# Kernel tuning notes

Hardware: AMD Instinct MI355X
Metric: run time of the kernel (lower is better)

The kernel has to match this reference:

```python
import jax, jax.numpy as jnp
import numpy as np

NUM_STAB = 1e-3  # numerical_stabilizer for relu kernel


def _relu_feature(x, proj):
    # x: [B, L, H, D], proj: [M, D] -> [B, L, H, M]
    ratio = 1.0 / jnp.sqrt(jnp.asarray(proj.shape[0], x.dtype))
    return jax.nn.relu(ratio * jnp.einsum('blhd,md->blhm', x, proj)) + NUM_STAB


def setup_inputs() -> dict:
    key = jax.random.key(0)
    k1, k2, k3, k4, k5 = jax.random.split(key, 5)
    B, L, H, D, M = 16, 576, 12, 64, 8  # L = length_of_side**2 = 24**2
    return {
        'query': jax.random.normal(k1, (B, L, H, D), dtype=jnp.float32),
        'key': jax.random.normal(k2, (B, L, H, D), dtype=jnp.float32),
        'value': jax.random.normal(k3, (B, L, H, D), dtype=jnp.float32),
        'projection_matrix': jax.random.normal(k4, (M, D), dtype=jnp.float32),
        # RPE mask is nonnegative per-head mixing matrix [H, L, L]
        'mask_matrix': jax.random.uniform(k5, (H, L, L), dtype=jnp.float32),
    }


def reference(query, key, value, projection_matrix, mask_matrix):
    # ReLU kernel features (projection_matrix_type='relu')
    q_prime = _relu_feature(query, projection_matrix)  # [B, L, H, M]
    k_prime = _relu_feature(key, projection_matrix)    # [B, L, H, M]
    B, L, H, M = k_prime.shape
    D = value.shape[-1]

    # D_1[b,l,h,m,d] = k'[b,l,h,m] * v[b,l,h,d], flattened over (m,d)
    D_1 = jnp.einsum('blhm,blhd->blhmd', k_prime, value).reshape(B, L, H, M * D)
    # mask-matrix causal/RPE mixing over the L dimension (per head)
    D_1_hat = jnp.einsum('hij,bjhc->bihc', mask_matrix, D_1).reshape(B, L, H, M, D)
    D_2_hat = jnp.einsum('hij,bjhm->bihm', mask_matrix, k_prime)  # [B, L, H, M]

    av_attention = jnp.einsum('blhm,blhmd->blhd', q_prime, D_1_hat)  # [B, L, H, D]
    ks_sum = jnp.sum(D_2_hat, axis=1)                                # [B, H, M]
    normalizer = jnp.einsum('blhm,bhm->blh', q_prime, ks_sum)        # [B, L, H]
    return av_attention / normalizer[..., None]
```

## Files before the change

### kernel.cpp

```cpp
#include <hip/hip_runtime.h>
#include <hip/hip_bf16.h>


#define B_ 16
#define L_ 576
#define H_ 12
#define D_ 64
#define M_ 8
#define NUM_STAB 1e-3f
#define RATIO 0.35355339059327373f

typedef __attribute__((ext_vector_type(8))) short short8;
typedef __attribute__((ext_vector_type(4))) float f32x4;

union Pack {
    uint4 u4;
    short8 s8;
    uint2 u2[2];
    unsigned u[4];
    unsigned short us[8];
};

__device__ inline unsigned short f2bf(float x) {
    union { float f; unsigned u; } a; a.f = x;
    unsigned r = (a.u + 0x7FFFu + ((a.u >> 16) & 1u)) >> 16;
    return (unsigned short)r;
}
__device__ inline unsigned pk2(float lo, float hi) {
    __hip_bfloat162 h = __float22bfloat162_rn(make_float2(lo, hi));
    union { __hip_bfloat162 b; unsigned u; } c; c.b = h;
    return c.u;
}
__device__ inline float bf2f(unsigned short u) {
    union { unsigned u; float f; } c; c.u = (unsigned)u << 16; return c.f;
}

#define WS_W_OFF  (H_ * L_)
#define WS_QP_OFF (H_ * L_ + B_ * H_ * M_)
#define QP_ELEMS  ((size_t)B_ * H_ * L_ * M_)

__global__ __launch_bounds__(256) void feat_kernel(const float* __restrict__ q,
                                                   const float* __restrict__ k,
                                                   const float* __restrict__ v,
                                                   const float* __restrict__ proj,
                                                   const float* __restrict__ mask,
                                                   unsigned short* __restrict__ qp,
                                                   unsigned short* __restrict__ kp,
                                                   float* __restrict__ cmask,
                                                   unsigned short* __restrict__ vt) {
    __shared__ float cred[4][16];
    const int lc = blockIdx.x, h = blockIdx.y, b = blockIdx.z, t = threadIdx.x;
    const int wv = t >> 6, l = t & 63, r8 = l >> 3, c8 = l & 7;
    const int row = lc * 32 + wv * 8 + r8;

    float4 pj0[8], pj1[8];
#pragma unroll
    for (int m = 0; m < 8; ++m) {
        pj0[m] = *(const float4*)(proj + m * 64 + c8 * 8);
        pj1[m] = *(const float4*)(proj + m * 64 + c8 * 8 + 4);
    }

#pragma unroll
    for (int s = 0; s < 2; ++s) {
        const float* src = s ? k : q;
        unsigned short* dst = s ? kp : qp;
        const float* xp = src + (((size_t)b * L_ + row) * H_ + h) * D_ + c8 * 8;
        float4 x0 = *(const float4*)xp;
        float4 x1 = *(const float4*)(xp + 4);
        x0.x *= RATIO; x0.y *= RATIO; x0.z *= RATIO; x0.w *= RATIO;
        x1.x *= RATIO; x1.y *= RATIO; x1.z *= RATIO; x1.w *= RATIO;
        float p[8];
#pragma unroll
        for (int m = 0; m < 8; ++m) {
            p[m] = x0.x * pj0[m].x + x0.y * pj0[m].y + x0.z * pj0[m].z + x0.w * pj0[m].w
                 + x1.x * pj1[m].x + x1.y * pj1[m].y + x1.z * pj1[m].z + x1.w * pj1[m].w;
        }
#pragma unroll
        for (int st = 1; st <= 4; st <<= 1) {
#pragma unroll
            for (int m = 0; m < 8; ++m) p[m] += __shfl_xor(p[m], st, 64);
        }
        float r = p[0];
        r = (c8 == 1) ? p[1] : r;
        r = (c8 == 2) ? p[2] : r;
        r = (c8 == 3) ? p[3] : r;
        r = (c8 == 4) ? p[4] : r;
        r = (c8 == 5) ? p[5] : r;
        r = (c8 == 6) ? p[6] : r;
        r = (c8 == 7) ? p[7] : r;
        r = fmaxf(r, 0.f) + NUM_STAB;
        dst[((size_t)(b * H_ + h) * L_ + row) * 8 + c8] = f2bf(r);
    }

    {
        const int dv = t >> 2;
        const int jl = (lc & 1) * 32 + (t & 3) * 8;
        const int jt9 = lc >> 1;
        const float* vsrc = v + (((size_t)b * L_ + jt9 * 64 + jl) * H_ + h) * D_ + dv;
        float tv[8];
#pragma unroll
        for (int e = 0; e < 8; ++e) tv[e] = vsrc[(size_t)e * (H_ * D_)];
        Pack pv;
#pragma unroll
        for (int q4 = 0; q4 < 4; ++q4) pv.u[q4] = pk2(tv[2 * q4], tv[2 * q4 + 1]);
        *(uint4*)&vt[((size_t)(b * H_ + h) * 9 + jt9) * 4096 + dv * 64 + jl] = pv.u4;
    }

    if (b < 2) {
        const int c = t & 15, rg = t >> 4;
        const int col0 = lc * 32 + b * 16;
        const float* mb = mask + (size_t)h * L_ * L_ + col0 + c;
        float a = 0.f;
#pragma unroll 4
        for (int k2 = 0; k2 < 36; ++k2) a += mb[(size_t)(rg + 16 * k2) * L_];
        a += __shfl_xor(a, 16, 64);
        a += __shfl_xor(a, 32, 64);
        if ((l >> 4) == 0) cred[wv][c] = a;
        __syncthreads();
        if (t < 16) cmask[h * L_ + col0 + t] = cred[0][t] + cred[1][t] + cred[2][t] + cred[3][t];
    }
}

__global__ __launch_bounds__(64) void wsum_kernel(const unsigned short* __restrict__ kp,
                                                  const float* __restrict__ cmask,
                                                  float* __restrict__ wbuf) {
    const int bh = blockIdx.x, lx = threadIdx.x;
    const int h = bh % H_;
    const unsigned short* kpb = kp + (size_t)bh * L_ * 8;
    const float* cm = cmask + h * L_;
    float a[8] = {0.f, 0.f, 0.f, 0.f, 0.f, 0.f, 0.f, 0.f};
    for (int j = lx; j < L_; j += 64) {
        const float c = cm[j];
        Pack pk; pk.u4 = *(const uint4*)(kpb + (size_t)j * 8);
#pragma unroll
        for (int m = 0; m < 8; ++m) a[m] += c * bf2f(pk.us[m]);
    }
#pragma unroll
    for (int st = 1; st < 64; st <<= 1) {
#pragma unroll
        for (int m = 0; m < 8; ++m) a[m] += __shfl_xor(a[m], st, 64);
    }
    float r = a[0];
    r = (lx == 1) ? a[1] : r;
    r = (lx == 2) ? a[2] : r;
    r = (lx == 3) ? a[3] : r;
    r = (lx == 4) ? a[4] : r;
    r = (lx == 5) ? a[5] : r;
    r = (lx == 6) ? a[6] : r;
    r = (lx == 7) ? a[7] : r;
    if (lx < 8) wbuf[(size_t)bh * 8 + lx] = r;
}

__global__ __launch_bounds__(256, 5) void attn_kernel(const float* __restrict__ mask,
                                                      const unsigned short* __restrict__ qp,
                                                      const unsigned short* __restrict__ kp,
                                                      const unsigned short* __restrict__ vt,
                                                      const float* __restrict__ wbuf,
                                                      float* __restrict__ out) {
    __shared__ __align__(16) unsigned short Sp[4 * 16 * 72];
    __shared__ __align__(16) unsigned short Bt[2][64 * 72];

    const int t = threadIdx.x;
    int id = blockIdx.x;
    const int bhi = id & 7; id >>= 3;
    const int blo = id & 1; id >>= 1;
    const int it = id % 9, h = id / 9;
    const int b = bhi * 2 + blo;
    const int i0 = it * 64;

    const int wv = t >> 6, l = t & 63, c15 = l & 15, kq = l >> 4;
    const int bd = t >> 3, bg = t & 7;
    const int vt_off = bd * 64 + bg * 8;

    const float* maskbase = mask + (size_t)h * L_ * L_ + (size_t)(i0 + 16 * wv + c15) * L_;
    const unsigned short* kpb = kp + (size_t)(b * H_ + h) * L_ * 8;
    const unsigned short* vtb = vt + (size_t)(b * H_ + h) * 9 * 4096;
    unsigned short* SpW = Sp + wv * 16 * 72;

    short8 Bq;
    {
        Pack pk; pk.u4 = make_uint4(0, 0, 0, 0);
        if (kq == 0)
            pk.u4 = *(const uint4*)(qp + ((size_t)(b * H_ + h) * L_ + i0 + 16 * wv + c15) * 8);
        Bq = pk.s8;
    }

    f32x4 acc0 = {0.f, 0.f, 0.f, 0.f}, acc1 = acc0, acc2 = acc0, acc3 = acc0;
    const f32x4 zz = {0.f, 0.f, 0.f, 0.f};

    uint4 a0 = make_uint4(0, 0, 0, 0), a1 = a0, a2 = a0, a3 = a0;
    uint4 vt0, vt1;
    float4 mv0, mv1, mv2, mv3;
    if (kq == 0) {
        a0 = *(const uint4*)(kpb + (size_t)(c15) * 8);
        a1 = *(const uint4*)(kpb + (size_t)(16 + c15) * 8);
        a2 = *(const uint4*)(kpb + (size_t)(32 + c15) * 8);
        a3 = *(const uint4*)(kpb + (size_t)(48 + c15) * 8);
    }
    vt0 = *(const uint4*)(vtb + vt_off);
    vt1 = *(const uint4*)(vtb + 2048 + vt_off);
    mv0 = *(const float4*)(maskbase + 0 + 4 * kq);
    mv1 = *(const float4*)(maskbase + 16 + 4 * kq);
    mv2 = *(const float4*)(maskbase + 32 + 4 * kq);
    mv3 = *(const float4*)(maskbase + 48 + 4 * kq);

    for (int jt = 0; jt < 9; ++jt) {
        const int slab = jt & 1;

        f32x4 s0, s1, s2, s3;
        {
            Pack p0, p1, p2, p3;
            p0.u4 = a0; p1.u4 = a1; p2.u4 = a2; p3.u4 = a3;
            s0 = __builtin_amdgcn_mfma_f32_16x16x32_bf16(p0.s8, Bq, zz, 0, 0, 0);
            s1 = __builtin_amdgcn_mfma_f32_16x16x32_bf16(p1.s8, Bq, zz, 0, 0, 0);
            s2 = __builtin_amdgcn_mfma_f32_16x16x32_bf16(p2.s8, Bq, zz, 0, 0, 0);
            s3 = __builtin_amdgcn_mfma_f32_16x16x32_bf16(p3.s8, Bq, zz, 0, 0, 0);
        }

        *(uint4*)&Bt[slab][bd * 72 + bg * 8] = vt0;
        *(uint4*)&Bt[slab][(bd + 32) * 72 + bg * 8] = vt1;

        {
            uint2 st2;
            st2.x = pk2(s0[0] * mv0.x, s0[1] * mv0.y);
            st2.y = pk2(s0[2] * mv0.z, s0[3] * mv0.w);
            *(uint2*)&SpW[c15 * 72 + 0 + 4 * kq] = st2;
            st2.x = pk2(s1[0] * mv1.x, s1[1] * mv1.y);
            st2.y = pk2(s1[2] * mv1.z, s1[3] * mv1.w);
            *(uint2*)&SpW[c15 * 72 + 16 + 4 * kq] = st2;
            st2.x = pk2(s2[0] * mv2.x, s2[1] * mv2.y);
            st2.y = pk2(s2[2] * mv2.z, s2[3] * mv2.w);
            *(uint2*)&SpW[c15 * 72 + 32 + 4 * kq] = st2;
            st2.x = pk2(s3[0] * mv3.x, s3[1] * mv3.y);
            st2.y = pk2(s3[2] * mv3.z, s3[3] * mv3.w);
            *(uint2*)&SpW[c15 * 72 + 48 + 4 * kq] = st2;
        }

        __syncthreads();

        {
            const int jn = (jt < 8) ? jt + 1 : 0;
            const int j0n = jn * 64;
            if (kq == 0) {
                a0 = *(const uint4*)(kpb + (size_t)(j0n + c15) * 8);
                a1 = *(const uint4*)(kpb + (size_t)(j0n + 16 + c15) * 8);
                a2 = *(const uint4*)(kpb + (size_t)(j0n + 32 + c15) * 8);
                a3 = *(const uint4*)(kpb + (size_t)(j0n + 48 + c15) * 8);
            }
            vt0 = *(const uint4*)(vtb + (size_t)jn * 4096 + vt_off);
            vt1 = *(const uint4*)(vtb + (size_t)jn * 4096 + 2048 + vt_off);
            mv0 = *(const float4*)(maskbase + j0n + 0 + 4 * kq);
            mv1 = *(const float4*)(maskbase + j0n + 16 + 4 * kq);
            mv2 = *(const float4*)(maskbase + j0n + 32 + 4 * kq);
            mv3 = *(const float4*)(maskbase + j0n + 48 + 4 * kq);
        }

        {
            short8 As0 = *(const short8*)&SpW[c15 * 72 + kq * 8];
            short8 As1 = *(const short8*)&SpW[c15 * 72 + 32 + kq * 8];
            const unsigned short* bp0 = &Bt[slab][c15 * 72 + kq * 8];
            const unsigned short* bp1 = bp0 + 16 * 72;
            const unsigned short* bp2 = bp0 + 32 * 72;
            const unsigned short* bp3 = bp0 + 48 * 72;
            acc0 = __builtin_amdgcn_mfma_f32_16x16x32_bf16(As0, *(const short8*)bp0, acc0, 0, 0, 0);
            acc0 = __builtin_amdgcn_mfma_f32_16x16x32_bf16(As1, *(const short8*)(bp0 + 32), acc0, 0, 0, 0);
            acc1 = __builtin_amdgcn_mfma_f32_16x16x32_bf16(As0, *(const short8*)bp1, acc1, 0, 0, 0);
            acc1 = __builtin_amdgcn_mfma_f32_16x16x32_bf16(As1, *(const short8*)(bp1 + 32), acc1, 0, 0, 0);
            acc2 = __builtin_amdgcn_mfma_f32_16x16x32_bf16(As0, *(const short8*)bp2, acc2, 0, 0, 0);
            acc2 = __builtin_amdgcn_mfma_f32_16x16x32_bf16(As1, *(const short8*)(bp2 + 32), acc2, 0, 0, 0);
            acc3 = __builtin_amdgcn_mfma_f32_16x16x32_bf16(As0, *(const short8*)bp3, acc3, 0, 0, 0);
            acc3 = __builtin_amdgcn_mfma_f32_16x16x32_bf16(As1, *(const short8*)(bp3 + 32), acc3, 0, 0, 0);
        }
    }

    const float* wp = wbuf + (size_t)(b * H_ + h) * 8;
    const float4 w0 = *(const float4*)wp;
    const float4 w1 = *(const float4*)(wp + 4);
    Pack pq;
    pq.u4 = *(const uint4*)(qp + ((size_t)(b * H_ + h) * L_ + i0 + 16 * wv + c15) * 8);
    float n = bf2f(pq.us[0]) * w0.x + bf2f(pq.us[1]) * w0.y +
              bf2f(pq.us[2]) * w0.z + bf2f(pq.us[3]) * w0.w +
              bf2f(pq.us[4]) * w1.x + bf2f(pq.us[5]) * w1.y +
              bf2f(pq.us[6]) * w1.z + bf2f(pq.us[7]) * w1.w;
    float iv[4];
#pragma unroll
    for (int r = 0; r < 4; ++r) iv[r] = 1.0f / __shfl(n, 4 * kq + r, 64);

    float* ob = out + (((size_t)b * L_ + i0 + 16 * wv + 4 * kq) * H_ + h) * D_ + c15;
    const f32x4 aa[4] = {acc0, acc1, acc2, acc3};
#pragma unroll
    for (int di = 0; di < 4; ++di)
#pragma unroll
        for (int r = 0; r < 4; ++r)
            ob[(size_t)r * (H_ * D_) + 16 * di] = aa[di][r] * iv[r];
}

extern "C" void kernel_launch(void* const* d_in, const int* in_sizes, int n_in,
                              void* d_out, int out_size, void* d_ws, size_t ws_size,
                              hipStream_t stream) {
    const float* q    = (const float*)d_in[0];
    const float* k    = (const float*)d_in[1];
    const float* v    = (const float*)d_in[2];
    const float* proj = (const float*)d_in[3];
    const float* mask = (const float*)d_in[4];
    float* out = (float*)d_out;

    float* ws = (float*)d_ws;
    float* cmask = ws;
    float* wbuf  = ws + WS_W_OFF;
    unsigned short* qp_w = (unsigned short*)(ws + WS_QP_OFF);
    unsigned short* kp_w = qp_w + QP_ELEMS;
    unsigned short* vt_w = kp_w + QP_ELEMS;

    feat_kernel<<<dim3(L_ / 32, H_, B_), 256, 0, stream>>>(q, k, v, proj, mask, qp_w, kp_w, cmask, vt_w);
    wsum_kernel<<<B_ * H_, 64, 0, stream>>>(kp_w, cmask, wbuf);
    attn_kernel<<<1728, 256, 0, stream>>>(mask, qp_w, kp_w, vt_w, wbuf, out);
}
```

Measured before the change: 192.6 us.

## Load V fragments directly from global into registers, drop shared staging and barrier

The V tile was previously staged through a double-buffered shared-memory slab with a block-wide barrier each iteration. Now each lane loads its MFMA B-operand fragments for V straight from global memory into registers and prefetches the next tile. This removes the per-iteration __syncthreads and the LDS traffic for V. The cost is more registers (occupancy hint lowered from 5 to 4) and V tiles reloaded redundantly by each of the four waves instead of once per block.

```diff
diff --git a/kernel.cpp b/kernel.cpp
--- a/kernel.cpp
+++ b/kernel.cpp
@@ -151,14 +151,13 @@
     if (lx < 8) wbuf[(size_t)bh * 8 + lx] = r;
 }
 
-__global__ __launch_bounds__(256, 5) void attn_kernel(const float* __restrict__ mask,
+__global__ __launch_bounds__(256, 4) void attn_kernel(const float* __restrict__ mask,
                                                       const unsigned short* __restrict__ qp,
                                                       const unsigned short* __restrict__ kp,
                                                       const unsigned short* __restrict__ vt,
                                                       const float* __restrict__ wbuf,
                                                       float* __restrict__ out) {
     __shared__ __align__(16) unsigned short Sp[4 * 16 * 72];
-    __shared__ __align__(16) unsigned short Bt[2][64 * 72];
 
     const int t = threadIdx.x;
     int id = blockIdx.x;
@@ -169,12 +168,10 @@
     const int i0 = it * 64;
 
     const int wv = t >> 6, l = t & 63, c15 = l & 15, kq = l >> 4;
-    const int bd = t >> 3, bg = t & 7;
-    const int vt_off = bd * 64 + bg * 8;
-
-    const float* maskbase = mask + (size_t)h * L_ * L_ + (size_t)(i0 + 16 * wv + c15) * L_;
+
+    const float* maskbase = mask + (size_t)h * L_ * L_ + (size_t)(i0 + 16 * wv + c15) * L_ + 4 * kq;
     const unsigned short* kpb = kp + (size_t)(b * H_ + h) * L_ * 8;
-    const unsigned short* vtb = vt + (size_t)(b * H_ + h) * 9 * 4096;
+    const unsigned short* vfb = vt + (size_t)(b * H_ + h) * 9 * 4096 + c15 * 64 + kq * 8;
     unsigned short* SpW = Sp + wv * 16 * 72;
 
     short8 Bq;
@@ -189,24 +186,27 @@
     const f32x4 zz = {0.f, 0.f, 0.f, 0.f};
 
     uint4 a0 = make_uint4(0, 0, 0, 0), a1 = a0, a2 = a0, a3 = a0;
-    uint4 vt0, vt1;
-    float4 mv0, mv1, mv2, mv3;
     if (kq == 0) {
         a0 = *(const uint4*)(kpb + (size_t)(c15) * 8);
         a1 = *(const uint4*)(kpb + (size_t)(16 + c15) * 8);
         a2 = *(const uint4*)(kpb + (size_t)(32 + c15) * 8);
         a3 = *(const uint4*)(kpb + (size_t)(48 + c15) * 8);
     }
-    vt0 = *(const uint4*)(vtb + vt_off);
-    vt1 = *(const uint4*)(vtb + 2048 + vt_off);
-    mv0 = *(const float4*)(maskbase + 0 + 4 * kq);
-    mv1 = *(const float4*)(maskbase + 16 + 4 * kq);
-    mv2 = *(const float4*)(maskbase + 32 + 4 * kq);
-    mv3 = *(const float4*)(maskbase + 48 + 4 * kq);
-
+    float4 mv0 = *(const float4*)(maskbase + 0);
+    float4 mv1 = *(const float4*)(maskbase + 16);
+    float4 mv2 = *(const float4*)(maskbase + 32);
+    float4 mv3 = *(const float4*)(maskbase + 48);
+    uint4 vb00 = *(const uint4*)(vfb + 0);
+    uint4 vb01 = *(const uint4*)(vfb + 32);
+    uint4 vb10 = *(const uint4*)(vfb + 1024);
+    uint4 vb11 = *(const uint4*)(vfb + 1024 + 32);
+    uint4 vb20 = *(const uint4*)(vfb + 2048);
+    uint4 vb21 = *(const uint4*)(vfb + 2048 + 32);
+    uint4 vb30 = *(const uint4*)(vfb + 3072);
+    uint4 vb31 = *(const uint4*)(vfb + 3072 + 32);
+
+#pragma unroll 1
     for (int jt = 0; jt < 9; ++jt) {
-        const int slab = jt & 1;
-
         f32x4 s0, s1, s2, s3;
         {
             Pack p0, p1, p2, p3;
@@ -217,8 +217,20 @@
             s3 = __builtin_amdgcn_mfma_f32_16x16x32_bf16(p3.s8, Bq, zz, 0, 0, 0);
         }
 
-        *(uint4*)&Bt[slab][bd * 72 + bg * 8] = vt0;
-        *(uint4*)&Bt[slab][(bd + 32) * 72 + bg * 8] = vt1;
+        const int jn = (jt < 8) ? jt + 1 : 0;
+        const int j0n = jn * 64;
+
+        uint4 na0 = make_uint4(0, 0, 0, 0), na1 = na0, na2 = na0, na3 = na0;
+        if (kq == 0) {
+            na0 = *(const uint4*)(kpb + (size_t)(j0n + c15) * 8);
+            na1 = *(const uint4*)(kpb + (size_t)(j0n + 16 + c15) * 8);
+            na2 = *(const uint4*)(kpb + (size_t)(j0n + 32 + c15) * 8);
+            na3 = *(const uint4*)(kpb + (size_t)(j0n + 48 + c15) * 8);
+        }
+        float4 nmv0 = *(const float4*)(maskbase + j0n + 0);
+        float4 nmv1 = *(const float4*)(maskbase + j0n + 16);
+        float4 nmv2 = *(const float4*)(maskbase + j0n + 32);
+        float4 nmv3 = *(const float4*)(maskbase + j0n + 48);
 
         {
             uint2 st2;
@@ -236,41 +248,36 @@
             *(uint2*)&SpW[c15 * 72 + 48 + 4 * kq] = st2;
         }
 
-        __syncthreads();
-
         {
-            const int jn = (jt < 8) ? jt + 1 : 0;
-            const int j0n = jn * 64;
-            if (kq == 0) {
-                a0 = *(const uint4*)(kpb + (size_t)(j0n + c15) * 8);
-                a1 = *(const uint4*)(kpb + (size_t)(j0n + 16 + c15) * 8);
-                a2 = *(const uint4*)(kpb + (size_t)(j0n + 32 + c15) * 8);
-                a3 = *(const uint4*)(kpb + (size_t)(j0n + 48 + c15) * 8);
-            }
-            vt0 = *(const uint4*)(vtb + (size_t)jn * 4096 + vt_off);
-            vt1 = *(const uint4*)(vtb + (size_t)jn * 4096 + 2048 + vt_off);
-            mv0 = *(const float4*)(maskbase + j0n + 0 + 4 * kq);
-            mv1 = *(const float4*)(maskbase + j0n + 16 + 4 * kq);
-            mv2 = *(const float4*)(maskbase + j0n + 32 + 4 * kq);
-            mv3 = *(const float4*)(maskbase + j0n + 48 + 4 * kq);
-        }
-
-        {
+            Pack b00, b01, b10, b11, b20, b21, b30, b31;
+            b00.u4 = vb00; b01.u4 = vb01; b10.u4 = vb10; b11.u4 = vb11;
+            b20.u4 = vb20; b21.u4 = vb21; b30.u4 = vb30; b31.u4 = vb31;
             short8 As0 = *(const short8*)&SpW[c15 * 72 + kq * 8];
             short8 As1 = *(const short8*)&SpW[c15 * 72 + 32 + kq * 8];
-            const unsigned short* bp0 = &Bt[slab][c15 * 72 + kq * 8];
-            const unsigned short* bp1 = bp0 + 16 * 72;
-            const unsigned short* bp2 = bp0 + 32 * 72;
-            const unsigned short* bp3 = bp0 + 48 * 72;
-            acc0 = __builtin_amdgcn_mfma_f32_16x16x32_bf16(As0, *(const short8*)bp0, acc0, 0, 0, 0);
-            acc0 = __builtin_amdgcn_mfma_f32_16x16x32_bf16(As1, *(const short8*)(bp0 + 32), acc0, 0, 0, 0);
-            acc1 = __builtin_amdgcn_mfma_f32_16x16x32_bf16(As0, *(const short8*)bp1, acc1, 0, 0, 0);
-            acc1 = __builtin_amdgcn_mfma_f32_16x16x32_bf16(As1, *(const short8*)(bp1 + 32), acc1, 0, 0, 0);
-            acc2 = __builtin_amdgcn_mfma_f32_16x16x32_bf16(As0, *(const short8*)bp2, acc2, 0, 0, 0);
-            acc2 = __builtin_amdgcn_mfma_f32_16x16x32_bf16(As1, *(const short8*)(bp2 + 32), acc2, 0, 0, 0);
-            acc3 = __builtin_amdgcn_mfma_f32_16x16x32_bf16(As0, *(const short8*)bp3, acc3, 0, 0, 0);
-            acc3 = __builtin_amdgcn_mfma_f32_16x16x32_bf16(As1, *(const short8*)(bp3 + 32), acc3, 0, 0, 0);
-        }
+            acc0 = __builtin_amdgcn_mfma_f32_16x16x32_bf16(As0, b00.s8, acc0, 0, 0, 0);
+            acc0 = __builtin_amdgcn_mfma_f32_16x16x32_bf16(As1, b01.s8, acc0, 0, 0, 0);
+            acc1 = __builtin_amdgcn_mfma_f32_16x16x32_bf16(As0, b10.s8, acc1, 0, 0, 0);
+            acc1 = __builtin_amdgcn_mfma_f32_16x16x32_bf16(As1, b11.s8, acc1, 0, 0, 0);
+            acc2 = __builtin_amdgcn_mfma_f32_16x16x32_bf16(As0, b20.s8, acc2, 0, 0, 0);
+            acc2 = __builtin_amdgcn_mfma_f32_16x16x32_bf16(As1, b21.s8, acc2, 0, 0, 0);
+            acc3 = __builtin_amdgcn_mfma_f32_16x16x32_bf16(As0, b30.s8, acc3, 0, 0, 0);
+            acc3 = __builtin_amdgcn_mfma_f32_16x16x32_bf16(As1, b31.s8, acc3, 0, 0, 0);
+        }
+
+        {
+            const unsigned short* vn = vfb + (size_t)jn * 4096;
+            vb00 = *(const uint4*)(vn + 0);
+            vb01 = *(const uint4*)(vn + 32);
+            vb10 = *(const uint4*)(vn + 1024);
+            vb11 = *(const uint4*)(vn + 1024 + 32);
+            vb20 = *(const uint4*)(vn + 2048);
+            vb21 = *(const uint4*)(vn + 2048 + 32);
+            vb30 = *(const uint4*)(vn + 3072);
+            vb31 = *(const uint4*)(vn + 3072 + 32);
+        }
+
+        a0 = na0; a1 = na1; a2 = na2; a3 = na3;
+        mv0 = nmv0; mv1 = nmv1; mv2 = nmv2; mv3 = nmv3;
     }
 
     const float* wp = wbuf + (size_t)(b * H_ + h) * 8;
```

Measured after the change: 240.5 us. 1.25x slower.

## Fuse V transpose/bf16 conversion into attention kernel with XOR-swizzled LDS

Applied to the files above, without the earlier changes.

Removes the V transpose-to-bf16 staging from the feature kernel and its global round trip. The attention kernel now loads fp32 V directly, converts it to bf16 and writes it transposed into LDS. Padded LDS rows are replaced by XOR-swizzled layouts to avoid bank conflicts, and s_setprio is placed around the MFMA groups. Occupancy hint is raised from 5 to 6. Each of the 1728 attention blocks rereads and reconverts V (fp32, twice the bytes) rather than reading a pre-packed tile, and the extra vf registers may pressure the higher occupancy target.

```diff
diff --git a/kernel.cpp b/kernel.cpp
--- a/kernel.cpp
+++ b/kernel.cpp
@@ -41,13 +41,11 @@
 
 __global__ __launch_bounds__(256) void feat_kernel(const float* __restrict__ q,
                                                    const float* __restrict__ k,
-                                                   const float* __restrict__ v,
                                                    const float* __restrict__ proj,
                                                    const float* __restrict__ mask,
                                                    unsigned short* __restrict__ qp,
                                                    unsigned short* __restrict__ kp,
-                                                   float* __restrict__ cmask,
-                                                   unsigned short* __restrict__ vt) {
+                                                   float* __restrict__ cmask) {
     __shared__ float cred[4][16];
     const int lc = blockIdx.x, h = blockIdx.y, b = blockIdx.z, t = threadIdx.x;
     const int wv = t >> 6, l = t & 63, r8 = l >> 3, c8 = l & 7;
@@ -90,20 +88,6 @@
         r = (c8 == 7) ? p[7] : r;
         r = fmaxf(r, 0.f) + NUM_STAB;
         dst[((size_t)(b * H_ + h) * L_ + row) * 8 + c8] = f2bf(r);
-    }
-
-    {
-        const int dv = t >> 2;
-        const int jl = (lc & 1) * 32 + (t & 3) * 8;
-        const int jt9 = lc >> 1;
-        const float* vsrc = v + (((size_t)b * L_ + jt9 * 64 + jl) * H_ + h) * D_ + dv;
-        float tv[8];
-#pragma unroll
-        for (int e = 0; e < 8; ++e) tv[e] = vsrc[(size_t)e * (H_ * D_)];
-        Pack pv;
-#pragma unroll
-        for (int q4 = 0; q4 < 4; ++q4) pv.u[q4] = pk2(tv[2 * q4], tv[2 * q4 + 1]);
-        *(uint4*)&vt[((size_t)(b * H_ + h) * 9 + jt9) * 4096 + dv * 64 + jl] = pv.u4;
     }
 
     if (b < 2) {
@@ -151,14 +135,14 @@
     if (lx < 8) wbuf[(size_t)bh * 8 + lx] = r;
 }
 
-__global__ __launch_bounds__(256, 5) void attn_kernel(const float* __restrict__ mask,
+__global__ __launch_bounds__(256, 6) void attn_kernel(const float* __restrict__ v,
+                                                      const float* __restrict__ mask,
                                                       const unsigned short* __restrict__ qp,
                                                       const unsigned short* __restrict__ kp,
-                                                      const unsigned short* __restrict__ vt,
                                                       const float* __restrict__ wbuf,
                                                       float* __restrict__ out) {
-    __shared__ __align__(16) unsigned short Sp[4 * 16 * 72];
-    __shared__ __align__(16) unsigned short Bt[2][64 * 72];
+    __shared__ __align__(16) unsigned short Sp[4 * 16 * 64];
+    __shared__ __align__(16) unsigned short Bt[2][64 * 64];
 
     const int t = threadIdx.x;
     int id = blockIdx.x;
@@ -169,13 +153,14 @@
     const int i0 = it * 64;
 
     const int wv = t >> 6, l = t & 63, c15 = l & 15, kq = l >> 4;
-    const int bd = t >> 3, bg = t & 7;
-    const int vt_off = bd * 64 + bg * 8;
-
-    const float* maskbase = mask + (size_t)h * L_ * L_ + (size_t)(i0 + 16 * wv + c15) * L_;
+
+    const float* maskbase = mask + (size_t)h * L_ * L_ + (size_t)(i0 + 16 * wv + c15) * L_ + 4 * kq;
     const unsigned short* kpb = kp + (size_t)(b * H_ + h) * L_ * 8;
-    const unsigned short* vtb = vt + (size_t)(b * H_ + h) * 9 * 4096;
-    unsigned short* SpW = Sp + wv * 16 * 72;
+    const float* vb = v + ((size_t)b * L_ * H_ + h) * D_ + l;
+
+    char* SpB = (char*)Sp + wv * 2048;
+    const int sxor = (c15 & 7) << 4;
+    const int lxor = (l & 7) << 4;
 
     short8 Bq;
     {
@@ -188,88 +173,100 @@
     f32x4 acc0 = {0.f, 0.f, 0.f, 0.f}, acc1 = acc0, acc2 = acc0, acc3 = acc0;
     const f32x4 zz = {0.f, 0.f, 0.f, 0.f};
 
+    float vf[16];
+    float4 mv0, mv1, mv2, mv3;
     uint4 a0 = make_uint4(0, 0, 0, 0), a1 = a0, a2 = a0, a3 = a0;
-    uint4 vt0, vt1;
-    float4 mv0, mv1, mv2, mv3;
-    if (kq == 0) {
-        a0 = *(const uint4*)(kpb + (size_t)(c15) * 8);
-        a1 = *(const uint4*)(kpb + (size_t)(16 + c15) * 8);
-        a2 = *(const uint4*)(kpb + (size_t)(32 + c15) * 8);
-        a3 = *(const uint4*)(kpb + (size_t)(48 + c15) * 8);
-    }
-    vt0 = *(const uint4*)(vtb + vt_off);
-    vt1 = *(const uint4*)(vtb + 2048 + vt_off);
-    mv0 = *(const float4*)(maskbase + 0 + 4 * kq);
-    mv1 = *(const float4*)(maskbase + 16 + 4 * kq);
-    mv2 = *(const float4*)(maskbase + 32 + 4 * kq);
-    mv3 = *(const float4*)(maskbase + 48 + 4 * kq);
+    {
+#pragma unroll
+        for (int qv = 0; qv < 16; ++qv) vf[qv] = vb[(size_t)(16 * wv + qv) * (H_ * D_)];
+        mv0 = *(const float4*)(maskbase + 0);
+        mv1 = *(const float4*)(maskbase + 16);
+        mv2 = *(const float4*)(maskbase + 32);
+        mv3 = *(const float4*)(maskbase + 48);
+        if (kq == 0) {
+            a0 = *(const uint4*)(kpb + (size_t)(c15) * 8);
+            a1 = *(const uint4*)(kpb + (size_t)(16 + c15) * 8);
+            a2 = *(const uint4*)(kpb + (size_t)(32 + c15) * 8);
+            a3 = *(const uint4*)(kpb + (size_t)(48 + c15) * 8);
+        }
+    }
 
     for (int jt = 0; jt < 9; ++jt) {
         const int slab = jt & 1;
+        char* BtB = (char*)Bt[slab];
 
         f32x4 s0, s1, s2, s3;
         {
             Pack p0, p1, p2, p3;
             p0.u4 = a0; p1.u4 = a1; p2.u4 = a2; p3.u4 = a3;
+            __builtin_amdgcn_s_setprio(1);
             s0 = __builtin_amdgcn_mfma_f32_16x16x32_bf16(p0.s8, Bq, zz, 0, 0, 0);
             s1 = __builtin_amdgcn_mfma_f32_16x16x32_bf16(p1.s8, Bq, zz, 0, 0, 0);
             s2 = __builtin_amdgcn_mfma_f32_16x16x32_bf16(p2.s8, Bq, zz, 0, 0, 0);
             s3 = __builtin_amdgcn_mfma_f32_16x16x32_bf16(p3.s8, Bq, zz, 0, 0, 0);
-        }
-
-        *(uint4*)&Bt[slab][bd * 72 + bg * 8] = vt0;
-        *(uint4*)&Bt[slab][(bd + 32) * 72 + bg * 8] = vt1;
-
-        {
+            __builtin_amdgcn_s_setprio(0);
+        }
+
+        {
+            Pack p0, p1;
+#pragma unroll
+            for (int qv = 0; qv < 4; ++qv) p0.u[qv] = pk2(vf[2 * qv], vf[2 * qv + 1]);
+#pragma unroll
+            for (int qv = 0; qv < 4; ++qv) p1.u[qv] = pk2(vf[8 + 2 * qv], vf[9 + 2 * qv]);
+            const int base = l * 128 + 32 * wv;
+            *(uint4*)(BtB + ((base) ^ lxor)) = p0.u4;
+            *(uint4*)(BtB + ((base + 16) ^ lxor)) = p1.u4;
+        }
+
+        {
+            const int sb = c15 * 128 + 8 * kq;
             uint2 st2;
             st2.x = pk2(s0[0] * mv0.x, s0[1] * mv0.y);
             st2.y = pk2(s0[2] * mv0.z, s0[3] * mv0.w);
-            *(uint2*)&SpW[c15 * 72 + 0 + 4 * kq] = st2;
+            *(uint2*)(SpB + ((sb + 0) ^ sxor)) = st2;
             st2.x = pk2(s1[0] * mv1.x, s1[1] * mv1.y);
             st2.y = pk2(s1[2] * mv1.z, s1[3] * mv1.w);
-            *(uint2*)&SpW[c15 * 72 + 16 + 4 * kq] = st2;
+            *(uint2*)(SpB + ((sb + 32) ^ sxor)) = st2;
             st2.x = pk2(s2[0] * mv2.x, s2[1] * mv2.y);
             st2.y = pk2(s2[2] * mv2.z, s2[3] * mv2.w);
-            *(uint2*)&SpW[c15 * 72 + 32 + 4 * kq] = st2;
+            *(uint2*)(SpB + ((sb + 64) ^ sxor)) = st2;
             st2.x = pk2(s3[0] * mv3.x, s3[1] * mv3.y);
             st2.y = pk2(s3[2] * mv3.z, s3[3] * mv3.w);
-            *(uint2*)&SpW[c15 * 72 + 48 + 4 * kq] = st2;
+            *(uint2*)(SpB + ((sb + 96) ^ sxor)) = st2;
         }
 
         __syncthreads();
 
         {
-            const int jn = (jt < 8) ? jt + 1 : 0;
-            const int j0n = jn * 64;
+            const int j0n = ((jt < 8) ? jt + 1 : 0) * 64;
+#pragma unroll
+            for (int qv = 0; qv < 16; ++qv) vf[qv] = vb[(size_t)(j0n + 16 * wv + qv) * (H_ * D_)];
+            mv0 = *(const float4*)(maskbase + j0n + 0);
+            mv1 = *(const float4*)(maskbase + j0n + 16);
+            mv2 = *(const float4*)(maskbase + j0n + 32);
+            mv3 = *(const float4*)(maskbase + j0n + 48);
             if (kq == 0) {
                 a0 = *(const uint4*)(kpb + (size_t)(j0n + c15) * 8);
                 a1 = *(const uint4*)(kpb + (size_t)(j0n + 16 + c15) * 8);
                 a2 = *(const uint4*)(kpb + (size_t)(j0n + 32 + c15) * 8);
                 a3 = *(const uint4*)(kpb + (size_t)(j0n + 48 + c15) * 8);
             }
-            vt0 = *(const uint4*)(vtb + (size_t)jn * 4096 + vt_off);
-            vt1 = *(const uint4*)(vtb + (size_t)jn * 4096 + 2048 + vt_off);
-            mv0 = *(const float4*)(maskbase + j0n + 0 + 4 * kq);
-            mv1 = *(const float4*)(maskbase + j0n + 16 + 4 * kq);
-            mv2 = *(const float4*)(maskbase + j0n + 32 + 4 * kq);
-            mv3 = *(const float4*)(maskbase + j0n + 48 + 4 * kq);
-        }
-
-        {
-            short8 As0 = *(const short8*)&SpW[c15 * 72 + kq * 8];
-            short8 As1 = *(const short8*)&SpW[c15 * 72 + 32 + kq * 8];
-            const unsigned short* bp0 = &Bt[slab][c15 * 72 + kq * 8];
-            const unsigned short* bp1 = bp0 + 16 * 72;
-            const unsigned short* bp2 = bp0 + 32 * 72;
-            const unsigned short* bp3 = bp0 + 48 * 72;
-            acc0 = __builtin_amdgcn_mfma_f32_16x16x32_bf16(As0, *(const short8*)bp0, acc0, 0, 0, 0);
-            acc0 = __builtin_amdgcn_mfma_f32_16x16x32_bf16(As1, *(const short8*)(bp0 + 32), acc0, 0, 0, 0);
-            acc1 = __builtin_amdgcn_mfma_f32_16x16x32_bf16(As0, *(const short8*)bp1, acc1, 0, 0, 0);
-            acc1 = __builtin_amdgcn_mfma_f32_16x16x32_bf16(As1, *(const short8*)(bp1 + 32), acc1, 0, 0, 0);
-            acc2 = __builtin_amdgcn_mfma_f32_16x16x32_bf16(As0, *(const short8*)bp2, acc2, 0, 0, 0);
-            acc2 = __builtin_amdgcn_mfma_f32_16x16x32_bf16(As1, *(const short8*)(bp2 + 32), acc2, 0, 0, 0);
-            acc3 = __builtin_amdgcn_mfma_f32_16x16x32_bf16(As0, *(const short8*)bp3, acc3, 0, 0, 0);
-            acc3 = __builtin_amdgcn_mfma_f32_16x16x32_bf16(As1, *(const short8*)(bp3 + 32), acc3, 0, 0, 0);
+        }
+
+        {
+            short8 As0 = *(const short8*)(SpB + ((c15 * 128 + 16 * kq) ^ sxor));
+            short8 As1 = *(const short8*)(SpB + ((c15 * 128 + 64 + 16 * kq) ^ sxor));
+            __builtin_amdgcn_s_setprio(1);
+#pragma unroll
+            for (int di = 0; di < 4; ++di) {
+                const int rb = (16 * di + c15) * 128;
+                short8 B0 = *(const short8*)(BtB + ((rb + 16 * kq) ^ sxor));
+                short8 B1 = *(const short8*)(BtB + ((rb + 64 + 16 * kq) ^ sxor));
+                f32x4* ap = (di == 0) ? &acc0 : (di == 1) ? &acc1 : (di == 2) ? &acc2 : &acc3;
+                *ap = __builtin_amdgcn_mfma_f32_16x16x32_bf16(As0, B0, *ap, 0, 0, 0);
+                *ap = __builtin_amdgcn_mfma_f32_16x16x32_bf16(As1, B1, *ap, 0, 0, 0);
+            }
+            __builtin_amdgcn_s_setprio(0);
         }
     }
 
@@ -310,9 +307,8 @@
     float* wbuf  = ws + WS_W_OFF;
     unsigned short* qp_w = (unsigned short*)(ws + WS_QP_OFF);
     unsigned short* kp_w = qp_w + QP_ELEMS;
-    unsigned short* vt_w = kp_w + QP_ELEMS;
-
-    feat_kernel<<<dim3(L_ / 32, H_, B_), 256, 0, stream>>>(q, k, v, proj, mask, qp_w, kp_w, cmask, vt_w);
+
+    feat_kernel<<<dim3(L_ / 32, H_, B_), 256, 0, stream>>>(q, k, proj, mask, qp_w, kp_w, cmask);
     wsum_kernel<<<B_ * H_, 64, 0, stream>>>(kp_w, cmask, wbuf);
-    attn_kernel<<<1728, 256, 0, stream>>>(mask, qp_w, kp_w, vt_w, wbuf, out);
-}
+    attn_kernel<<<1728, 256, 0, stream>>>(v, mask, qp_w, kp_w, wbuf, out);
+}
```

Result: slower. 276.4 us (+43.5%).
